# Optimization experiments

Measured on AMD Instinct MI355X. Metric: run time of the kernel, lower is better.

## Reference

```python
import jax, jax.numpy as jnp
import numpy as np

A_MIN = 0.001
EPS = 1e-08


def setup_inputs() -> dict:
    key = jax.random.key(0)
    k1, k2, k3, k4 = jax.random.split(key, 4)
    B, O, I = 512, 1024, 512
    x = jax.random.normal(k1, (B, I), dtype=jnp.float32)
    translation = jax.random.uniform(k2, (O, I), dtype=jnp.float32, minval=-1.0, maxval=1.0)
    scale_raw = jax.random.uniform(k3, (O, I), dtype=jnp.float32, minval=-2.0, maxval=0.0)
    weights = jax.random.normal(k4, (O, I), dtype=jnp.float32) * (1.0 / np.sqrt(I))
    return {"x": x, "translation": translation, "scale_raw": scale_raw, "weights": weights}


def reference(x, translation, scale_raw, weights):
    # x: (B, I); params: (O, I)
    scale = A_MIN + jax.nn.softplus(scale_raw)  # (O, I)
    # s: (B, O, I) broadcast intermediate
    s = (x[:, None, :] - translation[None, :, :]) / (scale[None, :, :] + EPS)
    s2 = s * s
    wavelet = (1.0 - s2) * jnp.exp(-0.5 * s2)  # mexican hat
    y = jnp.einsum('oi,boi->bo', weights, wavelet)  # reduce over in_features
    return y
```

## Files before the change

kernel.cpp:

```cpp
#include <hip/hip_runtime.h>
#include <hip/hip_bf16.h>


#define WL_A_MIN 0.001f
#define WL_EPS   1e-8f

constexpr int WL_B = 512;
constexpr int WL_O = 1024;
constexpr int WL_I = 512;

#define WL_SQK  0.84932180553704583800f
#define WL_IK   1.38629436111989061883f
#define WL_L2E  1.44269504088896340736f
#define WL_LN2  0.69314718055994530942f

typedef float v2f __attribute__((ext_vector_type(2)));

struct P3 { float nti, inv, w; };

__device__ __forceinline__ float fast_exp2(float a) {
#if __has_builtin(__builtin_amdgcn_exp2f)
    return __builtin_amdgcn_exp2f(a);
#else
    return exp2f(a);
#endif
}
__device__ __forceinline__ float fast_log2(float a) {
#if __has_builtin(__builtin_amdgcn_logf)
    return __builtin_amdgcn_logf(a);
#else
    return __log2f(a);
#endif
}
__device__ __forceinline__ float fast_rcp(float a) {
#if __has_builtin(__builtin_amdgcn_rcpf)
    return __builtin_amdgcn_rcpf(a);
#else
    return 1.0f / a;
#endif
}

__global__ __launch_bounds__(256) void wl_prep(
    const float* __restrict__ translation,
    const float* __restrict__ scale_raw,
    const float* __restrict__ weights,
    P3* __restrict__ pT3)
{
    const int lane   = threadIdx.x & 63;
    const int ic     = threadIdx.x >> 6;
    const int o      = blockIdx.x * 64 + lane;
    const int i_base = blockIdx.y * 64 + ic * 16;

    #pragma unroll 4
    for (int k = 0; k < 16; ++k) {
        int i  = i_base + k;
        int gi = o * WL_I + i;
        float t  = translation[gi];
        float sr = scale_raw[gi];
        float w  = weights[gi];
        float ex    = fast_exp2(sr * WL_L2E);
        float sp    = fast_log2(1.0f + ex) * WL_LN2;
        float inv   = fast_rcp(WL_A_MIN + sp + WL_EPS);
        float inv_s = inv * WL_SQK;
        P3 pv; pv.nti = -t * inv_s; pv.inv = inv_s; pv.w = w;
        pT3[(size_t)i * WL_O + o] = pv;
    }
}

constexpr int R_REG = 544;
constexpr int R_KS  = 68;

__global__ __launch_bounds__(256, 6) void wl_main(
    const float* __restrict__ x,
    const P3* __restrict__ pT3,
    float* __restrict__ out)
{
    __shared__ float smem[4 * R_REG];

    const int tid  = threadIdx.x;
    const int lane = tid & 63;
    const int wid  = tid >> 6;
    const int o    = blockIdx.x * 64 + lane;
    const int b0   = blockIdx.y * 4;

    #pragma unroll
    for (int c = 0; c < 2; ++c) {
        int i = c * 256 + tid;
        float4 v;
        v.x = x[(size_t)(b0 + 0) * WL_I + i];
        v.y = x[(size_t)(b0 + 1) * WL_I + i];
        v.z = x[(size_t)(b0 + 2) * WL_I + i];
        v.w = x[(size_t)(b0 + 3) * WL_I + i];
        *reinterpret_cast<float4*>(&smem[i * 4]) = v;
    }
    __syncthreads();

    const P3* pp = pT3 + o;

    v2f aE0 = {0.f, 0.f}, aE1 = {0.f, 0.f};
    v2f aU0 = {0.f, 0.f}, aU1 = {0.f, 0.f};

    const int iBeg = wid * 128;
    #pragma unroll 4
    for (int ii = 0; ii < 128; ++ii) {
        const int i = iBeg + ii;
        P3 p = pp[(size_t)i * WL_O];
        float4 xq = *reinterpret_cast<const float4*>(&smem[i * 4]);

        v2f nti = {p.nti, p.nti};
        v2f inv = {p.inv, p.inv};
        v2f wv  = {p.w,  p.w};

        v2f x01 = {xq.x, xq.y};
        v2f x23 = {xq.z, xq.w};

        v2f s0 = __builtin_elementwise_fma(x01, inv, nti);
        v2f s1 = __builtin_elementwise_fma(x23, inv, nti);
        v2f u0 = s0 * s0;
        v2f u1 = s1 * s1;
        v2f e0 = {fast_exp2(-u0.x), fast_exp2(-u0.y)};
        v2f e1 = {fast_exp2(-u1.x), fast_exp2(-u1.y)};
        aE0 = __builtin_elementwise_fma(wv, e0, aE0);
        aE1 = __builtin_elementwise_fma(wv, e1, aE1);
        v2f ue0 = u0 * e0;
        v2f ue1 = u1 * e1;
        aU0 = __builtin_elementwise_fma(wv, ue0, aU0);
        aU1 = __builtin_elementwise_fma(wv, ue1, aU1);
    }

    __syncthreads();
    {
        float* r = &smem[wid * R_REG + lane];
        r[0 * R_KS] = aE0.x; r[1 * R_KS] = aE0.y;
        r[2 * R_KS] = aE1.x; r[3 * R_KS] = aE1.y;
        r[4 * R_KS] = aU0.x; r[5 * R_KS] = aU0.y;
        r[6 * R_KS] = aU1.x; r[7 * R_KS] = aU1.y;
    }
    __syncthreads();
    if (wid == 0) {
        float E[4] = {0.f, 0.f, 0.f, 0.f};
        float U[4] = {0.f, 0.f, 0.f, 0.f};
        #pragma unroll
        for (int w = 0; w < 4; ++w) {
            const float* r = &smem[w * R_REG + lane];
            E[0] += r[0 * R_KS]; E[1] += r[1 * R_KS];
            E[2] += r[2 * R_KS]; E[3] += r[3 * R_KS];
            U[0] += r[4 * R_KS]; U[1] += r[5 * R_KS];
            U[2] += r[6 * R_KS]; U[3] += r[7 * R_KS];
        }
        #pragma unroll
        for (int k = 0; k < 4; ++k)
            out[(size_t)(b0 + k) * WL_O + o] = fmaf(-WL_IK, U[k], E[k]);
    }
}

extern "C" void kernel_launch(void* const* d_in, const int* in_sizes, int n_in,
                              void* d_out, int out_size, void* d_ws, size_t ws_size,
                              hipStream_t stream) {
    const float* x           = (const float*)d_in[0];
    const float* translation = (const float*)d_in[1];
    const float* scale_raw   = (const float*)d_in[2];
    const float* weights     = (const float*)d_in[3];
    float*       out         = (float*)d_out;
    P3*          pT3         = (P3*)d_ws;

    wl_prep<<<dim3(WL_O / 64, WL_I / 64), dim3(256), 0, stream>>>(
        translation, scale_raw, weights, pT3);

    wl_main<<<dim3(WL_O / 64, WL_B / 4), dim3(256), 0, stream>>>(x, pT3, out);
}
```

Measured before the change: 114.6 us.

## Compute wavelet inner loop in packed fp16 with fused mexican-hat term

Precomputed per-(i,o) parameters are stored as four fp16 values instead of three fp32 floats, and x is staged in shared memory as fp16. The hot loop now does the affine transform, square, exp2 and the (1 - k*u) factor in packed half-precision math, then accumulates into fp32. This lets a single accumulator per batch row replace the separate E and U accumulators. The aim is to cut memory traffic and ALU/transcendental cost per element, at the risk of fp16 error in s, u and exp that may exceed the output tolerance.

```diff
diff --git a/kernel.cpp b/kernel.cpp
--- a/kernel.cpp
+++ b/kernel.cpp
@@ -14,9 +14,8 @@
 #define WL_L2E  1.44269504088896340736f
 #define WL_LN2  0.69314718055994530942f
 
-typedef float v2f __attribute__((ext_vector_type(2)));
-
-struct P3 { float nti, inv, w; };
+typedef _Float16 h2 __attribute__((ext_vector_type(2)));
+typedef _Float16 h4 __attribute__((ext_vector_type(4)));
 
 __device__ __forceinline__ float fast_exp2(float a) {
 #if __has_builtin(__builtin_amdgcn_exp2f)
@@ -44,7 +43,7 @@
     const float* __restrict__ translation,
     const float* __restrict__ scale_raw,
     const float* __restrict__ weights,
-    P3* __restrict__ pT3)
+    h4* __restrict__ pT)
 {
     const int lane   = threadIdx.x & 63;
     const int ic     = threadIdx.x >> 6;
@@ -62,20 +61,24 @@
         float sp    = fast_log2(1.0f + ex) * WL_LN2;
         float inv   = fast_rcp(WL_A_MIN + sp + WL_EPS);
         float inv_s = inv * WL_SQK;
-        P3 pv; pv.nti = -t * inv_s; pv.inv = inv_s; pv.w = w;
-        pT3[(size_t)i * WL_O + o] = pv;
+        h4 pv;
+        pv.x = (_Float16)(-t * inv_s);
+        pv.y = (_Float16)inv_s;
+        pv.z = (_Float16)w;
+        pv.w = (_Float16)0.0f;
+        pT[(size_t)i * WL_O + o] = pv;
     }
 }
 
-constexpr int R_REG = 544;
 constexpr int R_KS  = 68;
+constexpr int R_REG = 4 * R_KS;
 
 __global__ __launch_bounds__(256, 6) void wl_main(
     const float* __restrict__ x,
-    const P3* __restrict__ pT3,
+    const h4* __restrict__ pT,
     float* __restrict__ out)
 {
-    __shared__ float smem[4 * R_REG];
+    __shared__ float smem[1280];
 
     const int tid  = threadIdx.x;
     const int lane = tid & 63;
@@ -86,71 +89,68 @@
     #pragma unroll
     for (int c = 0; c < 2; ++c) {
         int i = c * 256 + tid;
-        float4 v;
-        v.x = x[(size_t)(b0 + 0) * WL_I + i];
-        v.y = x[(size_t)(b0 + 1) * WL_I + i];
-        v.z = x[(size_t)(b0 + 2) * WL_I + i];
-        v.w = x[(size_t)(b0 + 3) * WL_I + i];
-        *reinterpret_cast<float4*>(&smem[i * 4]) = v;
+        float a0 = x[(size_t)(b0 + 0) * WL_I + i];
+        float a1 = x[(size_t)(b0 + 1) * WL_I + i];
+        float a2 = x[(size_t)(b0 + 2) * WL_I + i];
+        float a3 = x[(size_t)(b0 + 3) * WL_I + i];
+        h4 v = {(_Float16)a0, (_Float16)a1, (_Float16)a2, (_Float16)a3};
+        *reinterpret_cast<h4*>(&smem[i * 2]) = v;
     }
     __syncthreads();
 
-    const P3* pp = pT3 + o;
+    const h4* pp = pT + o;
+    const h2* xt = reinterpret_cast<const h2*>(smem);
 
-    v2f aE0 = {0.f, 0.f}, aE1 = {0.f, 0.f};
-    v2f aU0 = {0.f, 0.f}, aU1 = {0.f, 0.f};
+    float a0 = 0.f, a1 = 0.f, a2 = 0.f, a3 = 0.f;
+    const h2 one2 = {(_Float16)1.0f, (_Float16)1.0f};
+    const h2 nIK2 = {(_Float16)(-WL_IK), (_Float16)(-WL_IK)};
 
     const int iBeg = wid * 128;
-    #pragma unroll 4
+    #pragma unroll 8
     for (int ii = 0; ii < 128; ++ii) {
         const int i = iBeg + ii;
-        P3 p = pp[(size_t)i * WL_O];
-        float4 xq = *reinterpret_cast<const float4*>(&smem[i * 4]);
+        h4 p  = pp[(size_t)i * WL_O];
+        h2 xA = xt[i * 2];
+        h2 xB = xt[i * 2 + 1];
 
-        v2f nti = {p.nti, p.nti};
-        v2f inv = {p.inv, p.inv};
-        v2f wv  = {p.w,  p.w};
+        h2 nti2 = {p.x, p.x};
+        h2 inv2 = {p.y, p.y};
 
-        v2f x01 = {xq.x, xq.y};
-        v2f x23 = {xq.z, xq.w};
+        h2 sA = __builtin_elementwise_fma(xA, inv2, nti2);
+        h2 sB = __builtin_elementwise_fma(xB, inv2, nti2);
+        h2 uA = sA * sA;
+        h2 uB = sB * sB;
+        h2 eA = __builtin_elementwise_exp2(-uA);
+        h2 eB = __builtin_elementwise_exp2(-uB);
+        h2 tA = __builtin_elementwise_fma(uA, nIK2, one2);
+        h2 tB = __builtin_elementwise_fma(uB, nIK2, one2);
+        h2 gA = eA * tA;
+        h2 gB = eB * tB;
 
-        v2f s0 = __builtin_elementwise_fma(x01, inv, nti);
-        v2f s1 = __builtin_elementwise_fma(x23, inv, nti);
-        v2f u0 = s0 * s0;
-        v2f u1 = s1 * s1;
-        v2f e0 = {fast_exp2(-u0.x), fast_exp2(-u0.y)};
-        v2f e1 = {fast_exp2(-u1.x), fast_exp2(-u1.y)};
-        aE0 = __builtin_elementwise_fma(wv, e0, aE0);
-        aE1 = __builtin_elementwise_fma(wv, e1, aE1);
-        v2f ue0 = u0 * e0;
-        v2f ue1 = u1 * e1;
-        aU0 = __builtin_elementwise_fma(wv, ue0, aU0);
-        aU1 = __builtin_elementwise_fma(wv, ue1, aU1);
+        a0 = fmaf((float)p.z, (float)gA.x, a0);
+        a1 = fmaf((float)p.z, (float)gA.y, a1);
+        a2 = fmaf((float)p.z, (float)gB.x, a2);
+        a3 = fmaf((float)p.z, (float)gB.y, a3);
     }
 
     __syncthreads();
-    {
-        float* r = &smem[wid * R_REG + lane];
-        r[0 * R_KS] = aE0.x; r[1 * R_KS] = aE0.y;
-        r[2 * R_KS] = aE1.x; r[3 * R_KS] = aE1.y;
-        r[4 * R_KS] = aU0.x; r[5 * R_KS] = aU0.y;
-        r[6 * R_KS] = aU1.x; r[7 * R_KS] = aU1.y;
+    if (wid != 0) {
+        float* r = &smem[(wid - 1) * R_REG + lane];
+        r[0 * R_KS] = a0; r[1 * R_KS] = a1;
+        r[2 * R_KS] = a2; r[3 * R_KS] = a3;
     }
     __syncthreads();
     if (wid == 0) {
-        float E[4] = {0.f, 0.f, 0.f, 0.f};
-        float U[4] = {0.f, 0.f, 0.f, 0.f};
         #pragma unroll
-        for (int w = 0; w < 4; ++w) {
-            const float* r = &smem[w * R_REG + lane];
-            E[0] += r[0 * R_KS]; E[1] += r[1 * R_KS];
-            E[2] += r[2 * R_KS]; E[3] += r[3 * R_KS];
-            U[0] += r[4 * R_KS]; U[1] += r[5 * R_KS];
-            U[2] += r[6 * R_KS]; U[3] += r[7 * R_KS];
+        for (int q = 0; q < 3; ++q) {
+            const float* r = &smem[q * R_REG + lane];
+            a0 += r[0 * R_KS]; a1 += r[1 * R_KS];
+            a2 += r[2 * R_KS]; a3 += r[3 * R_KS];
         }
-        #pragma unroll
-        for (int k = 0; k < 4; ++k)
-            out[(size_t)(b0 + k) * WL_O + o] = fmaf(-WL_IK, U[k], E[k]);
+        out[(size_t)(b0 + 0) * WL_O + o] = a0;
+        out[(size_t)(b0 + 1) * WL_O + o] = a1;
+        out[(size_t)(b0 + 2) * WL_O + o] = a2;
+        out[(size_t)(b0 + 3) * WL_O + o] = a3;
     }
 }
 
@@ -162,10 +162,10 @@
     const float* scale_raw   = (const float*)d_in[2];
     const float* weights     = (const float*)d_in[3];
     float*       out         = (float*)d_out;
-    P3*          pT3         = (P3*)d_ws;
+    h4*          pT          = (h4*)d_ws;
 
     wl_prep<<<dim3(WL_O / 64, WL_I / 64), dim3(256), 0, stream>>>(
-        translation, scale_raw, weights, pT3);
+        translation, scale_raw, weights, pT);
 
-    wl_main<<<dim3(WL_O / 64, WL_B / 4), dim3(256), 0, stream>>>(x, pT3, out);
+    wl_main<<<dim3(WL_O / 64, WL_B / 4), dim3(256), 0, stream>>>(x, pT, out);
 }
```

After: 120.5 us. 5.1% more time.
